# Optimization experiments

Hardware: AMD Instinct MI355X
Metric: run time of the kernel (lower is better)

The kernel has to match this reference:

```python
import jax, jax.numpy as jnp
import numpy as np

B, C, H, W = 8, 64, 128, 128
NH, OPH = 4, 16
MX, MY = 32, 17  # n_modes=(32,32) -> modes_y = 32//2+1
NPAT_S, NPAT_F = 10000, 5000
ED_S, ED_F = 64, 32


def setup_inputs() -> dict:
    ks = jax.random.split(jax.random.key(0), 16)
    n = lambda k, s, sc=1.0: jax.random.normal(k, s, dtype=jnp.float32) * sc
    z = lambda s: jnp.zeros(s, jnp.float32)
    return dict(
        x=n(ks[0], (B, C, H, W)),
        se_emb=n(ks[1], (NPAT_S, ED_S)),
        se_w=n(ks[2], (ED_S, C), 0.1), se_b=z(C),
        mhf_wr=n(ks[3], (NH, C, OPH, MX, MY), 0.01),
        mhf_wi=n(ks[4], (NH, C, OPH, MX, MY), 0.01),
        mhf_bias=z(C),
        sp_emb=n(ks[5], (NPAT_F, ED_F)),
        sp_wr=n(ks[6], (ED_F, C * MX * MY), 0.05), sp_br=z(C * MX * MY),
        sp_wi=n(ks[7], (ED_F, C * MX * MY), 0.05), sp_bi=z(C * MX * MY),
        gate_w1=n(ks[8], (3 * C, 64), 0.05), gate_b1=z(64),
        gate_w2=n(ks[9], (64, 3), 0.05), gate_b2=z(3),
        skip_w=n(ks[10], (C, C), 0.05), skip_b=z(C),
        norm_g=jnp.ones(C), norm_b=z(C),
        mlp_w1=n(ks[11], (C, 2 * C), 0.05), mlp_b1=z(2 * C),
        mlp_w2=n(ks[12], (2 * C, C), 0.05), mlp_b2=z(C),
    )


def _gelu(v):
    return jax.nn.gelu(v, approximate=False)


def _block(x, se_emb, se_w, se_b, mhf_wr, mhf_wi, mhf_bias, sp_emb, sp_wr, sp_br,
           sp_wi, sp_bi, gate_w1, gate_b1, gate_w2, gate_b2, skip_w, skip_b,
           norm_g, norm_b, mlp_w1, mlp_b1, mlp_w2, mlp_b2):
    Bq, Cq, Hq, Wq = x.shape
    # --- SpatialEngram: quantization is elementwise, so sum over window entries
    # equals 3x3 box-sum of the quantized padded field (identical integers,
    # avoids materializing the (B,C,H,W,3,3) unfold tensor).
    xp = jnp.pad(x, ((0, 0), (0, 0), (1, 1), (1, 1)), mode='edge')
    q = (xp * 100.0).astype(jnp.int32)  # trunc toward zero, same as torch .long()
    hv = jnp.zeros((Bq, Cq, Hq, Wq), jnp.int32)
    for i in range(3):
        for j in range(3):
            hv = hv + q[:, :, i:i + Hq, j:j + Wq]
    idx = (jnp.abs(hv) % NPAT_S).astype(jnp.float32).mean(axis=1).astype(jnp.int32)  # (B,H,W)
    spatial = jnp.moveaxis(se_emb[idx] @ se_w + se_b, -1, 1)  # (B,C,H,W)
    # --- MHF multi-head spectral conv (all heads in one einsum; concat == reshape)
    xf = jnp.fft.rfft2(x, norm='ortho')          # (B,C,H,W//2+1) complex64
    lo = xf[:, :, :MX, :MY]
    wc = (mhf_wr + 1j * mhf_wi).astype(lo.dtype)
    of = jnp.einsum('biXY,hioXY->bhoXY', lo, wc).reshape(Bq, Cq, MX, MY)
    full = jnp.zeros((Bq, Cq, Hq, Wq // 2 + 1), lo.dtype).at[:, :, :MX, :MY].set(of)
    mhf = jnp.fft.irfft2(full, s=(Hq, Wq), norm='ortho') + mhf_bias[:, None, None]
    # --- SpectralEngram: per-sample hash of low-freq magnitude -> embedding -> freq proj
    mag = jnp.abs(lo).mean(axis=(1, 2, 3))                       # (B,)
    fidx = (mag * 1000.0).astype(jnp.int32) % NPAT_F
    fe = sp_emb[fidx]                                            # (B,ED_F)
    re = (fe @ sp_wr + sp_br).reshape(Bq, Cq, MX, MY)
    im = (fe @ sp_wi + sp_bi).reshape(Bq, Cq, MX, MY)
    full2 = jnp.zeros((Bq, Cq, Hq, Wq // 2 + 1), lo.dtype).at[:, :, :MX, :MY].set(re + 1j * im)
    spec = jnp.fft.irfft2(full2, s=(Hq, Wq), norm='ortho')
    # --- gated fusion
    gate_in = jnp.concatenate([spatial.mean((2, 3)), mhf.mean((2, 3)), spec.mean((2, 3))], axis=-1)
    gw = jax.nn.softmax(_gelu(gate_in @ gate_w1 + gate_b1) @ gate_w2 + gate_b2, axis=-1)
    a = gw[:, 0, None, None, None]
    bt = gw[:, 1, None, None, None]
    gm = gw[:, 2, None, None, None]
    fused = a * spatial + bt * mhf + gm * spec
    y = fused + jnp.einsum('bihw,io->bohw', x, skip_w) + skip_b[:, None, None]
    # --- GroupNorm(1,C) + 1x1-conv channel MLP (dropout=0)
    mu = y.mean((1, 2, 3), keepdims=True)
    var = y.var((1, 2, 3), keepdims=True)
    yn = (y - mu) * jax.lax.rsqrt(var + 1e-5) * norm_g[:, None, None] + norm_b[:, None, None]
    h = _gelu(jnp.einsum('bihw,io->bohw', yn, mlp_w1) + mlp_b1[:, None, None])
    h = jnp.einsum('bihw,io->bohw', h, mlp_w2) + mlp_b2[:, None, None]
    return y + h


def reference(x, se_emb, se_w, se_b, mhf_wr, mhf_wi, mhf_bias, sp_emb, sp_wr, sp_br,
              sp_wi, sp_bi, gate_w1, gate_b1, gate_w2, gate_b2, skip_w, skip_b,
              norm_g, norm_b, mlp_w1, mlp_b1, mlp_w2, mlp_b2):
    return _block(x, se_emb, se_w, se_b, mhf_wr, mhf_wi, mhf_bias, sp_emb, sp_wr, sp_br,
                  sp_wi, sp_bi, gate_w1, gate_b1, gate_w2, gate_b2, skip_w, skip_b,
                  norm_g, norm_b, mlp_w1, mlp_b1, mlp_w2, mlp_b2)
```

## Files before the change

### kernel.cpp

```cpp
#include <hip/hip_runtime.h>
#include <hip/hip_bf16.h>
#include <math.h>

#define B_ 8
#define C_ 64
#define H_ 128
#define W_ 128
#define NH_ 4
#define OPH_ 16
#define MX_ 32
#define MY_ 17
#define NPAT_F 5000
#define ED_F 32
#define XY_ (MX_*MY_)
#define HW_ (H_*W_)
#define NE_ (B_*C_*H_*W_)

#define OFF_LO     0u
#define OFF_T1     2228224u
#define OFF_T2     2228224u
#define OFF_FMHF   11141120u
#define OFF_FSPEC  13369344u
#define OFF_IDX    33030144u

typedef __hip_bfloat16 bf16;

template<typename T>
__device__ __forceinline__ float ldt(const void* p, int i){ return (float)(((const T*)p)[i]); }

template<typename T>
__device__ __forceinline__ float2 ld2(const void* p, int i){
  if(sizeof(T)==4) return *(const float2*)((const float*)p + i);
  unsigned raw = *(const unsigned*)((const unsigned short*)p + i);
  return make_float2(__uint_as_float(raw<<16), __uint_as_float(raw & 0xffff0000u));
}

__device__ __forceinline__ float gelu_f(float a){
  return 0.5f*a*(1.0f + erff(a*0.70710678118654752f));
}

__device__ __forceinline__ int detect_f32(const void* ng){
  return (((const unsigned*)ng)[0] == 0x3F800000u) ? 1 : 0;
}

template<typename T>
__device__ __forceinline__ void hash_body(const void* x, int* idx, int b, int h, int w){
  int hm = h>0 ? h-1 : 0, hp = h<127 ? h+1 : 127;
  int wm = w>0 ? w-1 : 0, wp = w<127 ? w+1 : 127;
  int s = 0;
  for(int c=0;c<C_;++c){
    const int base = ((b*C_+c)*H_)*W_;
    const int r0 = base + hm*W_, r1 = base + h*W_, r2 = base + hp*W_;
    int q = (int)(ldt<T>(x,r0+wm)*100.0f) + (int)(ldt<T>(x,r0+w)*100.0f) + (int)(ldt<T>(x,r0+wp)*100.0f)
          + (int)(ldt<T>(x,r1+wm)*100.0f) + (int)(ldt<T>(x,r1+w)*100.0f) + (int)(ldt<T>(x,r1+wp)*100.0f)
          + (int)(ldt<T>(x,r2+wm)*100.0f) + (int)(ldt<T>(x,r2+w)*100.0f) + (int)(ldt<T>(x,r2+wp)*100.0f);
    s += (q < 0 ? -q : q) % 10000;
  }
  idx[(b*H_+h)*W_+w] = s >> 6;
}

__global__ __launch_bounds__(256) void k_xprep(const void* __restrict__ x, double* __restrict__ t1,
                                               const void* ng, double* __restrict__ dmag,
                                               float* __restrict__ smean, float* __restrict__ ssum,
                                               float* __restrict__ ssq, int* __restrict__ idx){
  __shared__ float4 xs4[2048];
  __shared__ double2 csd[128];
  int t = threadIdx.x;
  int bid = blockIdx.x;
  int f = detect_f32(ng);
  if(bid == 0){
    if(t < 8){ dmag[t] = 0.0; ssum[t] = 0.f; ssq[t] = 0.f; }
    smean[t] = 0.f; smean[t+256] = 0.f;
  }
  if(bid < 1024){
    if(t<128){ double a = (double)t * (6.283185307179586476925286766559/128.0); csd[t] = make_double2(cos(a), sin(a)); }
    int h0 = (bid & 1) << 6, bcl = bid >> 1;
    long xbase = ((long)bcl*H_ + h0)*W_;
    if(f){
      const float4* xp = (const float4*)((const float*)x + xbase);
      for(int i=t;i<2048;i+=256){
        int r=i>>5, s=i&31;
        xs4[(r<<5) + (s ^ (r&31))] = xp[i];
      }
    } else {
      const uint2* xp = (const uint2*)((const unsigned short*)x + xbase);
      for(int i=t;i<2048;i+=256){
        int r=i>>5, s=i&31;
        uint2 raw = xp[i];
        xs4[(r<<5) + (s ^ (r&31))] = make_float4(
          __uint_as_float(raw.x<<16), __uint_as_float(raw.x & 0xffff0000u),
          __uint_as_float(raw.y<<16), __uint_as_float(raw.y & 0xffff0000u));
      }
    }
    __syncthreads();
    for(int o=t;o<MY_*64;o+=256){
      int ky = o>>6, hr = o&63;
      const float4* xr = xs4 + (hr<<5);
      const int sx = hr & 31;
      double ar=0.0, ai=0.0;
      int m = 0;
      for(int s=0;s<32;++s){
        float4 v4 = xr[s ^ sx];
        double2 c0 = csd[m]; ar = fma((double)v4.x, c0.x, ar); ai = fma(-(double)v4.x, c0.y, ai); m=(m+ky)&127;
        double2 c1 = csd[m]; ar = fma((double)v4.y, c1.x, ar); ai = fma(-(double)v4.y, c1.y, ai); m=(m+ky)&127;
        double2 c2 = csd[m]; ar = fma((double)v4.z, c2.x, ar); ai = fma(-(double)v4.z, c2.y, ai); m=(m+ky)&127;
        double2 c3 = csd[m]; ar = fma((double)v4.w, c3.x, ar); ai = fma(-(double)v4.w, c3.y, ai); m=(m+ky)&127;
      }
      long tt = ((long)(bcl*MY_ + ky))*H_ + (h0 + hr);
      *(double2*)(t1 + 2*tt) = make_double2(ar, ai);
    }
  } else {
    int hb = bid - 1024;
    int b = hb >> 6, h = ((hb & 63) << 1) + (t >> 7), w = t & 127;
    if(f) hash_body<float>(x, idx, b, h, w); else hash_body<bf16>(x, idx, b, h, w);
  }
}

__global__ __launch_bounds__(576) void k_f2m(const double* __restrict__ t1, float* __restrict__ lo,
                                             double* __restrict__ dmag){
  __shared__ double2 ts[MY_*129];
  __shared__ double2 csd[128];
  __shared__ double sred[9];
  int t = threadIdx.x;
  if(t<128){ double a = (double)t * (6.283185307179586476925286766559/128.0); csd[t] = make_double2(cos(a), sin(a)); }
  int bcl = blockIdx.x;
  const double2* tg = (const double2*)t1 + (size_t)bcl*MY_*H_;
  for(int i=t;i<MY_*H_;i+=576){ int ky=i>>7, hh=i&127; ts[ky*129+hh] = tg[i]; }
  __syncthreads();
  double s = 0.0;
  if(t < 544){
    int ky = t % MY_, kx = t / MY_;
    const double2* tr = ts + ky*129;
    double ar=0.0, ai=0.0;
    int m = 0;
    for(int h=0;h<H_;++h){
      double2 v = tr[h];
      double2 cs2 = csd[m];
      double vr = v.x, vi = v.y;
      double cc = cs2.x, ss = cs2.y;
      ar += vr*cc + vi*ss;
      ai += vi*cc - vr*ss;
      m = (m + kx) & 127;
    }
    int g = bcl*XY_ + kx*MY_ + ky;
    float fr = (float)(ar*(1.0/128.0)), fi = (float)(ai*(1.0/128.0));
    *(float2*)(lo + 2*g) = make_float2(fr, fi);
    double re = (double)fr, im = (double)fi;
    s = sqrt(re*re + im*im);
  }
  for(int off=32; off; off>>=1) s += __shfl_down(s, off);
  if((t & 63) == 0) sred[t >> 6] = s;
  __syncthreads();
  if(t == 0){
    double tot = 0.0;
    #pragma unroll
    for(int i=0;i<9;++i) tot += sred[i];
    atomicAdd(&dmag[bcl >> 6], tot);
  }
}

template<typename T>
__device__ __forceinline__ void spatial_load_w(const void* se_w, const void* se_b, float wsm[64][64], float* sb, int t){
  for(int i=t;i<4096;i+=256) wsm[i>>6][i&63] = ldt<T>(se_w, i);
  if(t<64) sb[t] = ldt<T>(se_b, t);
}
template<typename T>
__device__ __forceinline__ void spatial_load_emb(const void* se_emb, const int* ibs, float* emb, int w0, int t){
  for(int i=t;i<2048;i+=256){ int wl_=i>>6, e=i&63; emb[wl_*68 + e] = ldt<T>(se_emb, ibs[w0+wl_]*64 + e); }
}
__global__ __launch_bounds__(256) void k_spatial(const void* se_emb, const void* se_w, const void* se_b,
                                                 const int* __restrict__ idx, bf16* __restrict__ spatial,
                                                 float* __restrict__ smean, const void* ng){
  __shared__ float wsm[64][64];
  __shared__ float emb[32*68];
  __shared__ float sb[64];
  __shared__ int ibs[128];
  int b = blockIdx.x >> 7, h = blockIdx.x & 127, t = threadIdx.x;
  int f = detect_f32(ng);
  if(f) spatial_load_w<float>(se_w, se_b, wsm, sb, t); else spatial_load_w<bf16>(se_w, se_b, wsm, sb, t);
  if(t<128) ibs[t] = idx[(b*H_+h)*W_ + t];
  __syncthreads();
  const int tx = t & 15, ty = t >> 4;
  const int c0 = ty << 2;
  float gsum[4] = {0.f, 0.f, 0.f, 0.f};
  for(int chunk=0; chunk<4; ++chunk){
    int w0 = chunk*32;
    if(f) spatial_load_emb<float>(se_emb, ibs, emb, w0, t); else spatial_load_emb<bf16>(se_emb, ibs, emb, w0, t);
    __syncthreads();
    float acc0[4], acc1[4];
    #pragma unroll
    for(int j=0;j<4;++j){ acc0[j]=sb[c0+j]; acc1[j]=sb[c0+j]; }
    #pragma unroll
    for(int e=0;e<64;e+=4){
      float4 ea = *(const float4*)(emb + tx*68 + e);
      float4 eb = *(const float4*)(emb + (tx+16)*68 + e);
      float ea4[4] = {ea.x, ea.y, ea.z, ea.w};
      float eb4[4] = {eb.x, eb.y, eb.z, eb.w};
      #pragma unroll
      for(int d=0;d<4;++d){
        float4 wv = *(const float4*)(&wsm[e+d][c0]);
        float w4[4] = {wv.x, wv.y, wv.z, wv.w};
        #pragma unroll
        for(int j=0;j<4;++j){
          acc0[j] = fmaf(ea4[d], w4[j], acc0[j]);
          acc1[j] = fmaf(eb4[d], w4[j], acc1[j]);
        }
      }
    }
    #pragma unroll
    for(int j=0;j<4;++j){
      int cc = c0 + j;
      int gb = ((b*C_+cc)*H_+h)*W_ + w0;
      bf16 v0 = __float2bfloat16(acc0[j]);
      bf16 v1 = __float2bfloat16(acc1[j]);
      spatial[gb + tx]      = v0;
      spatial[gb + tx + 16] = v1;
      gsum[j] += __bfloat162float(v0) + __bfloat162float(v1);
    }
    __syncthreads();
  }
  #pragma unroll
  for(int j=0;j<4;++j){
    float g2 = gsum[j];
    g2 += __shfl_xor(g2, 1); g2 += __shfl_xor(g2, 2);
    g2 += __shfl_xor(g2, 4); g2 += __shfl_xor(g2, 8);
    if(tx == 0) atomicAdd(&smean[b*C_ + c0 + j], g2 * (1.0f/16384.0f));
  }
}

template<typename T>
__device__ __forceinline__ void mhf_body(const float* lp, const void* wr, const void* wi,
                                         float* fmhf, int b, int co){
  int hh = co >> 4, o = co & 15;
  for(int xy = threadIdx.x; xy < XY_; xy += 256){
    float ar=0.f, ai=0.f;
    for(int i=0;i<C_;++i){
      float2 l2 = *(const float2*)(lp + (i*XY_+xy)*2);
      float lr = l2.x, li = l2.y;
      int widx = ((hh*C_ + i)*OPH_ + o)*XY_ + xy;
      float wre = ldt<T>(wr, widx), wim = ldt<T>(wi, widx);
      ar += lr*wre - li*wim;
      ai += lr*wim + li*wre;
    }
    int oo = (b*C_ + co)*XY_ + xy;
    *(float2*)(fmhf + 2*oo) = make_float2(ar, ai);
  }
}
template<typename T>
__device__ __forceinline__ void specf_body(const void* sp_emb, const void* sp_wr, const void* sp_br,
                                           const void* sp_wi, const void* sp_bi, const double* dmag,
                                           float* fspec, float* fe, int b, int j0, int t){
  double mag = dmag[b] / (double)(C_*XY_);
  int fv = ((int)(mag*1000.0)) % NPAT_F;
  fv = fv < 0 ? 0 : (fv >= NPAT_F ? NPAT_F-1 : fv);
  if(t < ED_F) fe[t] = ldt<T>(sp_emb, fv*ED_F + t);
  __syncthreads();
  float2 rr = ld2<T>(sp_br, j0), ii = ld2<T>(sp_bi, j0);
  float re0=rr.x, re1=rr.y, im0=ii.x, im1=ii.y;
  #pragma unroll 8
  for(int e=0;e<ED_F;++e){
    float f = fe[e];
    float2 wr = ld2<T>(sp_wr, e*(C_*XY_)+j0);
    float2 wi = ld2<T>(sp_wi, e*(C_*XY_)+j0);
    re0 = fmaf(f, wr.x, re0); im0 = fmaf(f, wi.x, im0);
    re1 = fmaf(f, wr.y, re1); im1 = fmaf(f, wi.y, im1);
  }
  int o = b*C_*XY_ + j0;
  *(float4*)(fspec + 2*o) = make_float4(re0, im0, re1, im1);
}
__global__ __launch_bounds__(256) void k_msf(const float* __restrict__ lo, const void* wr, const void* wi,
                                             float* __restrict__ fmhf,
                                             const void* sp_emb, const void* sp_wr, const void* sp_br,
                                             const void* sp_wi, const void* sp_bi,
                                             const double* __restrict__ dmag,
                                             float* __restrict__ fspec, const void* ng){
  __shared__ float fe[ED_F];
  int bid = blockIdx.x;
  int f = detect_f32(ng);
  if(bid < 512){
    int xcd = bid & 7, slot = bid >> 3;
    int co = (xcd << 3) + (slot & 7);
    int b  = slot >> 3;
    const float* lp = lo + b*C_*XY_*2;
    if(f) mhf_body<float>(lp, wr, wi, fmhf, b, co); else mhf_body<bf16>(lp, wr, wi, fmhf, b, co);
  } else {
    int sidx = bid - 512;
    int b = sidx / 68;
    int j0 = ((sidx % 68)*256 + threadIdx.x)*2;
    if(f) specf_body<float>(sp_emb, sp_wr, sp_br, sp_wi, sp_bi, dmag, fspec, fe, b, j0, threadIdx.x);
    else  specf_body<bf16 >(sp_emb, sp_wr, sp_br, sp_wi, sp_bi, dmag, fspec, fe, b, j0, threadIdx.x);
  }
}

template<typename T>
__device__ __forceinline__ void gate_calc(const float* smean, const float* fmhf, const float* fspec,
                                          const void* mbias, const void* w1, const void* b1,
                                          const void* w2, const void* b2,
                                          float* gin, float* hid, float* gwsh, int b, int t){
  if(t < 64){
    gin[t]      = smean[b*C_+t];
    gin[64+t]   = fmhf [(b*C_+t)*XY_*2] * (1.0f/128.0f) + ldt<T>(mbias, t);
    gin[128+t]  = fspec[(b*C_+t)*XY_*2] * (1.0f/128.0f);
  }
  __syncthreads();
  if(t < 64){
    float acc = ldt<T>(b1, t);
    for(int k=0;k<192;++k) acc = fmaf(gin[k], ldt<T>(w1, k*64+t), acc);
    hid[t] = gelu_f(acc);
  }
  __syncthreads();
  if(t==0){
    float o[3];
    for(int j=0;j<3;++j){
      float a = ldt<T>(b2, j);
      for(int k=0;k<64;++k) a += hid[k]*ldt<T>(w2, k*3+j);
      o[j]=a;
    }
    float mx = fmaxf(o[0], fmaxf(o[1], o[2]));
    float e0=expf(o[0]-mx), e1=expf(o[1]-mx), e2=expf(o[2]-mx);
    float sum=e0+e1+e2;
    gwsh[0]=e0/sum; gwsh[1]=e1/sum; gwsh[2]=e2/sum;
  }
}
__global__ __launch_bounds__(256) void k_comb(const float* __restrict__ fmhf, const float* __restrict__ fspec,
                                              const float* __restrict__ smean, const void* mbias,
                                              const void* gw1, const void* gb1, const void* gw2, const void* gb2,
                                              float* __restrict__ gw, float* __restrict__ t2, const void* ng){
  __shared__ float Gr[XY_], Gi[XY_], cs[128], sn[128];
  __shared__ float gin[192];
  __shared__ float hid[64];
  __shared__ float gwsh[3];
  int c = blockIdx.x, b = blockIdx.y, t = threadIdx.x;
  int f = detect_f32(ng);
  if(t<128) __sincosf((float)t * 0.04908738521234052f, &sn[t], &cs[t]);
  if(f) gate_calc<float>(smean, fmhf, fspec, mbias, gw1, gb1, gw2, gb2, gin, hid, gwsh, b, t);
  else  gate_calc<bf16 >(smean, fmhf, fspec, mbias, gw1, gb1, gw2, gb2, gin, hid, gwsh, b, t);
  __syncthreads();
  float bt=gwsh[1], gm=gwsh[2];
  if(c==0 && t<3) gw[b*3+t] = gwsh[t];
  for(int i=t;i<XY_;i+=256){
    int o = ((b*C_+c)*XY_+i)*2;
    float2 fm = *(const float2*)(fmhf + o);
    float2 fs = *(const float2*)(fspec + o);
    Gr[i] = bt*fm.x + gm*fs.x;
    Gi[i] = bt*fm.y + gm*fs.y;
  }
  __syncthreads();
  const int hh = t & 127;
  float cr[32], sr[32];
  #pragma unroll
  for(int kx=0;kx<MX_;++kx){ int m=(kx*hh)&127; cr[kx]=cs[m]; sr[kx]=sn[m]; }
  for(int i=t;i<MY_*H_;i+=256){
    int ky = i >> 7;
    float ar=0.f, ai=0.f;
    #pragma unroll 8
    for(int kx=0;kx<MX_;++kx){
      float fr=Gr[kx*MY_+ky], fi=Gi[kx*MY_+ky];
      ar += fr*cr[kx] - fi*sr[kx];
      ai += fr*sr[kx] + fi*cr[kx];
    }
    int e = (((b*C_+c)*MY_+ky)*H_ + hh)*2;
    *(float2*)(t2 + e) = make_float2(ar, ai);
  }
}

template<typename T>
__device__ __forceinline__ void fuse_body(const void* x, const void* skw, const void* skb, const void* mbias,
                                          bf16* sp_y, const float* t2, const float* gw,
                                          float* ssum, float* ssq,
                                          float wl[64][64], float* Ur0, float (*UrT)[16], float (*UiT)[16],
                                          float* cs, float* sn, float* sb, float* mb,
                                          float* s1, float* s2, int b, int h, int t){
  int w = t & 127, half = t >> 7;
  if(t<128) __sincosf((float)t * 0.04908738521234052f, &sn[t], &cs[t]);
  for(int i=t;i<4096;i+=256) wl[i>>6][i&63] = ldt<T>(skw, i);
  if(t<64){ sb[t]=ldt<T>(skb,t); mb[t]=ldt<T>(mbias,t); }
  for(int i=t;i<C_*MY_;i+=256){
    int cc=i/MY_, ky=i%MY_;
    int e = (((b*C_+cc)*MY_+ky)*H_ + h)*2;
    float2 v = *(const float2*)(t2 + e);
    if(ky==0){ Ur0[cc]=v.x; }
    else { UrT[cc][ky-1]=v.x; UiT[cc][ky-1]=v.y; }
  }
  float ga=gw[b*3], gbv=gw[b*3+1];
  __syncthreads();
  float cw[MY_], sw[MY_];
  #pragma unroll
  for(int ky=1;ky<MY_;++ky){ int m=(ky*w)&127; cw[ky]=cs[m]; sw[ky]=sn[m]; }
  int c0 = half*32;
  float acc[32];
  #pragma unroll
  for(int j=0;j<32;++j) acc[j]=sb[c0+j];
  int xb = (b*C_*H_ + h)*W_ + w;
  for(int k=0;k<64;++k){
    float xv = ldt<T>(x, xb + k*HW_);
    #pragma unroll
    for(int j=0;j<32;++j) acc[j] = fmaf(xv, wl[k][c0+j], acc[j]);
  }
  float ls=0.f, lq=0.f;
  for(int j=0;j<32;++j){
    int cc=c0+j;
    float vr = Ur0[cc];
    float4 ur0 = *(const float4*)(&UrT[cc][0]);
    float4 ur1 = *(const float4*)(&UrT[cc][4]);
    float4 ur2 = *(const float4*)(&UrT[cc][8]);
    float4 ur3 = *(const float4*)(&UrT[cc][12]);
    float4 ui0 = *(const float4*)(&UiT[cc][0]);
    float4 ui1 = *(const float4*)(&UiT[cc][4]);
    float4 ui2 = *(const float4*)(&UiT[cc][8]);
    float4 ui3 = *(const float4*)(&UiT[cc][12]);
    vr += 2.0f*(ur0.x*cw[1]  - ui0.x*sw[1]);
    vr += 2.0f*(ur0.y*cw[2]  - ui0.y*sw[2]);
    vr += 2.0f*(ur0.z*cw[3]  - ui0.z*sw[3]);
    vr += 2.0f*(ur0.w*cw[4]  - ui0.w*sw[4]);
    vr += 2.0f*(ur1.x*cw[5]  - ui1.x*sw[5]);
    vr += 2.0f*(ur1.y*cw[6]  - ui1.y*sw[6]);
    vr += 2.0f*(ur1.z*cw[7]  - ui1.z*sw[7]);
    vr += 2.0f*(ur1.w*cw[8]  - ui1.w*sw[8]);
    vr += 2.0f*(ur2.x*cw[9]  - ui2.x*sw[9]);
    vr += 2.0f*(ur2.y*cw[10] - ui2.y*sw[10]);
    vr += 2.0f*(ur2.z*cw[11] - ui2.z*sw[11]);
    vr += 2.0f*(ur2.w*cw[12] - ui2.w*sw[12]);
    vr += 2.0f*(ur3.x*cw[13] - ui3.x*sw[13]);
    vr += 2.0f*(ur3.y*cw[14] - ui3.y*sw[14]);
    vr += 2.0f*(ur3.z*cw[15] - ui3.z*sw[15]);
    vr += 2.0f*(ur3.w*cw[16] - ui3.w*sw[16]);
    int gi = ((b*C_+cc)*H_+h)*W_+w;
    float v = ga*__bfloat162float(sp_y[gi]) + vr*(1.0f/128.0f) + gbv*mb[cc] + acc[j];
    sp_y[gi] = __float2bfloat16(v);
    ls += v; lq = fmaf(v, v, lq);
  }
  s1[t]=ls; s2[t]=lq; __syncthreads();
  for(int k=128;k>0;k>>=1){ if(t<k){ s1[t]+=s1[t+k]; s2[t]+=s2[t+k]; } __syncthreads(); }
  if(t==0){ atomicAdd(&ssum[b], s1[0]); atomicAdd(&ssq[b], s2[0]); }
}
__global__ __launch_bounds__(256) void k_fuse(const void* x, const void* skw, const void* skb, const void* mbias,
                                              bf16* __restrict__ sp_y, const float* __restrict__ t2,
                                              const float* __restrict__ gw,
                                              float* __restrict__ ssum, float* __restrict__ ssq, const void* ng){
  __shared__ float wl[64][64];
  __shared__ float Ur0[64];
  __shared__ float UrT[64][16], UiT[64][16];
  __shared__ float cs[128], sn[128];
  __shared__ float sb[64], mb[64];
  __shared__ float s1[256], s2[256];
  int h = blockIdx.x, b = blockIdx.y, t = threadIdx.x;
  int f = detect_f32(ng);
  if(f) fuse_body<float>(x, skw, skb, mbias, sp_y, t2, gw, ssum, ssq, wl, Ur0, UrT, UiT, cs, sn, sb, mb, s1, s2, b, h, t);
  else  fuse_body<bf16 >(x, skw, skb, mbias, sp_y, t2, gw, ssum, ssq, wl, Ur0, UrT, UiT, cs, sn, sb, mb, s1, s2, b, h, t);
}

template<typename T>
__device__ __forceinline__ void mlp_body(const bf16* __restrict__ y, float mu, float rs,
                                         const void* ng, const void* nb, const void* w1, const void* b1,
                                         const void* w2, const void* b2, float* __restrict__ out,
                                         float* __restrict__ yn_s, float* __restrict__ w_s,
                                         int b, int h, int t){
  const int tx = t & 15, ty = t >> 4;
  const int pA = tx << 2, pB = 64 + (tx << 2);
  const int ybase = (b*C_*H_ + h)*W_;

  #pragma unroll
  for(int jj=0;jj<16;++jj) w_s[t + (jj<<8)] = ldt<T>(w1, t + (jj<<8));
  for(int it=0; it<8; ++it){
    int chunk = t + (it<<8);
    int c = chunk >> 5, p4 = (chunk & 31) << 2;
    const unsigned short* yp = (const unsigned short*)y + ybase + c*HW_ + p4;
    uint2 raw = *(const uint2*)yp;
    float g = ldt<T>(ng, c), nbv = ldt<T>(nb, c);
    float sc = rs*g;
    float4 o;
    o.x = (__uint_as_float(raw.x<<16)          - mu)*sc + nbv;
    o.y = (__uint_as_float(raw.x & 0xffff0000u)- mu)*sc + nbv;
    o.z = (__uint_as_float(raw.y<<16)          - mu)*sc + nbv;
    o.w = (__uint_as_float(raw.y & 0xffff0000u)- mu)*sc + nbv;
    *(float4*)(yn_s + c*132 + p4) = o;
  }
  float pf[16];
  #pragma unroll
  for(int jj=0;jj<16;++jj) pf[jj] = ldt<T>(w1, 4096 + t + (jj<<8));
  __syncthreads();

  const int kA = ty << 2, kB = 64 + (ty << 2);
  float a[8][8];
  #pragma unroll
  for(int j=0;j<4;++j){
    float bj = ldt<T>(b1, kA+j);
    float bj2 = ldt<T>(b1, kB+j);
    #pragma unroll
    for(int q=0;q<8;++q){ a[j][q]=bj; a[4+j][q]=bj2; }
  }
  #pragma unroll 4
  for(int i=0;i<32;++i){
    float4 y1 = *(const float4*)(yn_s + i*132 + pA);
    float4 y2 = *(const float4*)(yn_s + i*132 + pB);
    float4 wa = *(const float4*)(w_s + (i<<7) + kA);
    float4 wb = *(const float4*)(w_s + (i<<7) + kB);
    float y8[8] = {y1.x,y1.y,y1.z,y1.w,y2.x,y2.y,y2.z,y2.w};
    float w8[8] = {wa.x,wa.y,wa.z,wa.w,wb.x,wb.y,wb.z,wb.w};
    #pragma unroll
    for(int j=0;j<8;++j){
      #pragma unroll
      for(int q=0;q<8;++q) a[j][q] = fmaf(y8[q], w8[j], a[j][q]);
    }
  }
  __syncthreads();
  #pragma unroll
  for(int jj=0;jj<16;++jj) w_s[t + (jj<<8)] = pf[jj];
  #pragma unroll
  for(int jj=0;jj<16;++jj) pf[jj] = ldt<T>(w2, t + (jj<<8));
  __syncthreads();
  #pragma unroll 4
  for(int i=0;i<32;++i){
    float4 y1 = *(const float4*)(yn_s + (32+i)*132 + pA);
    float4 y2 = *(const float4*)(yn_s + (32+i)*132 + pB);
    float4 wa = *(const float4*)(w_s + (i<<7) + kA);
    float4 wb = *(const float4*)(w_s + (i<<7) + kB);
    float y8[8] = {y1.x,y1.y,y1.z,y1.w,y2.x,y2.y,y2.z,y2.w};
    float w8[8] = {wa.x,wa.y,wa.z,wa.w,wb.x,wb.y,wb.z,wb.w};
    #pragma unroll
    for(int j=0;j<8;++j){
      #pragma unroll
      for(int q=0;q<8;++q) a[j][q] = fmaf(y8[q], w8[j], a[j][q]);
    }
  }
  __syncthreads();
  #pragma unroll
  for(int jj=0;jj<16;++jj) w_s[t + (jj<<8)] = pf[jj];
  #pragma unroll
  for(int jj=0;jj<16;++jj) pf[jj] = ldt<T>(w2, 4096 + t + (jj<<8));
  #pragma unroll
  for(int j=0;j<4;++j){
    float4 h1, h2;
    h1.x = gelu_f(a[j][0]); h1.y = gelu_f(a[j][1]); h1.z = gelu_f(a[j][2]); h1.w = gelu_f(a[j][3]);
    h2.x = gelu_f(a[j][4]); h2.y = gelu_f(a[j][5]); h2.z = gelu_f(a[j][6]); h2.w = gelu_f(a[j][7]);
    *(float4*)(yn_s + (kA+j)*132 + pA) = h1;
    *(float4*)(yn_s + (kA+j)*132 + pB) = h2;
  }
  __syncthreads();

  const int c0 = ty << 2;
  float acc[4][8];
  #pragma unroll
  for(int j=0;j<4;++j){
    #pragma unroll
    for(int q=0;q<8;++q) acc[j][q] = 0.f;
  }
  #pragma unroll 4
  for(int k=0;k<64;++k){
    float4 h1 = *(const float4*)(yn_s + k*132 + pA);
    float4 h2 = *(const float4*)(yn_s + k*132 + pB);
    float4 wv = *(const float4*)(w_s + (k<<6) + c0);
    float h8[8] = {h1.x,h1.y,h1.z,h1.w,h2.x,h2.y,h2.z,h2.w};
    float w4[4] = {wv.x, wv.y, wv.z, wv.w};
    #pragma unroll
    for(int j=0;j<4;++j){
      #pragma unroll
      for(int q=0;q<8;++q) acc[j][q] = fmaf(h8[q], w4[j], acc[j][q]);
    }
  }
  __syncthreads();
  #pragma unroll
  for(int jj=0;jj<16;++jj) w_s[t + (jj<<8)] = pf[jj];
  #pragma unroll
  for(int j=0;j<4;++j){
    float4 h1, h2;
    h1.x = gelu_f(a[4+j][0]); h1.y = gelu_f(a[4+j][1]); h1.z = gelu_f(a[4+j][2]); h1.w = gelu_f(a[4+j][3]);
    h2.x = gelu_f(a[4+j][4]); h2.y = gelu_f(a[4+j][5]); h2.z = gelu_f(a[4+j][6]); h2.w = gelu_f(a[4+j][7]);
    *(float4*)(yn_s + (kA+j)*132 + pA) = h1;
    *(float4*)(yn_s + (kA+j)*132 + pB) = h2;
  }
  __syncthreads();
  #pragma unroll 4
  for(int k=0;k<64;++k){
    float4 h1 = *(const float4*)(yn_s + k*132 + pA);
    float4 h2 = *(const float4*)(yn_s + k*132 + pB);
    float4 wv = *(const float4*)(w_s + (k<<6) + c0);
    float h8[8] = {h1.x,h1.y,h1.z,h1.w,h2.x,h2.y,h2.z,h2.w};
    float w4[4] = {wv.x, wv.y, wv.z, wv.w};
    #pragma unroll
    for(int j=0;j<4;++j){
      #pragma unroll
      for(int q=0;q<8;++q) acc[j][q] = fmaf(h8[q], w4[j], acc[j][q]);
    }
  }

  #pragma unroll
  for(int j=0;j<4;++j){
    int c = c0 + j;
    float b2v = ldt<T>(b2, c);
    const unsigned short* yp1 = (const unsigned short*)y + ybase + c*HW_ + pA;
    const unsigned short* yp2 = (const unsigned short*)y + ybase + c*HW_ + pB;
    uint2 r1 = *(const uint2*)yp1;
    uint2 r2 = *(const uint2*)yp2;
    float4 o1, o2;
    o1.x = __uint_as_float(r1.x<<16)           + acc[j][0] + b2v;
    o1.y = __uint_as_float(r1.x & 0xffff0000u) + acc[j][1] + b2v;
    o1.z = __uint_as_float(r1.y<<16)           + acc[j][2] + b2v;
    o1.w = __uint_as_float(r1.y & 0xffff0000u) + acc[j][3] + b2v;
    o2.x = __uint_as_float(r2.x<<16)           + acc[j][4] + b2v;
    o2.y = __uint_as_float(r2.x & 0xffff0000u) + acc[j][5] + b2v;
    o2.z = __uint_as_float(r2.y<<16)           + acc[j][6] + b2v;
    o2.w = __uint_as_float(r2.y & 0xffff0000u) + acc[j][7] + b2v;
    *(float4*)(out + ybase + c*HW_ + pA) = o1;
    *(float4*)(out + ybase + c*HW_ + pB) = o2;
  }
}
__global__ __launch_bounds__(256) void k_mlp(const bf16* __restrict__ y, const float* __restrict__ ssum,
                                             const float* __restrict__ ssq, const void* ng, const void* nb,
                                             const void* w1, const void* b1, const void* w2, const void* b2,
                                             float* __restrict__ out){
  __shared__ float yn_s[64*132];
  __shared__ float w_s[4096];
  int h = blockIdx.x, b = blockIdx.y;
  int t = threadIdx.x;
  float m = ssum[b] * (1.0f/1048576.0f);
  float v = ssq[b] * (1.0f/1048576.0f) - m*m;
  float rs = rsqrtf(v + 1e-5f);
  int f = detect_f32(ng);
  if(f) mlp_body<float>(y, m, rs, ng, nb, w1, b1, w2, b2, out, yn_s, w_s, b, h, t);
  else  mlp_body<bf16 >(y, m, rs, ng, nb, w1, b1, w2, b2, out, yn_s, w_s, b, h, t);
}

extern "C" void kernel_launch(void* const* d_in, const int* in_sizes, int n_in,
                              void* d_out, int out_size, void* d_ws, size_t ws_size,
                              hipStream_t stream) {
  (void)out_size; (void)ws_size;
  static const int dict_sizes[24] = {8388608,640000,4096,64,2228224,2228224,64,160000,
                                     1114112,34816,1114112,34816,12288,64,192,3,
                                     4096,64,64,64,8192,128,8192,64};
  static const int sorted_sizes[24] = {64,3,12288,192,64,2228224,2228224,128,64,8192,8192,
                                       64,64,64,640000,4096,64,4096,34816,34816,160000,
                                       1114112,1114112,8388608};
  static const int sorted_to_dict[24] = {13,15,12,14,6,5,4,21,23,20,22,19,18,3,1,2,17,16,11,9,7,10,8,0};

  const void* in[24];
  bool is_dict = (n_in == 24), is_sorted = (n_in == 24);
  if(n_in == 24){
    for(int i=0;i<24;++i){
      if(in_sizes[i] != dict_sizes[i])   is_dict   = false;
      if(in_sizes[i] != sorted_sizes[i]) is_sorted = false;
    }
  }
  if(is_sorted && !is_dict){
    for(int i=0;i<24;++i) in[sorted_to_dict[i]] = d_in[i];
  } else {
    for(int i=0;i<24 && i<n_in;++i) in[i] = d_in[i];
  }

  const void* x       = in[0];
  const void* se_emb  = in[1];
  const void* se_w    = in[2];
  const void* se_b    = in[3];
  const void* mhf_wr  = in[4];
  const void* mhf_wi  = in[5];
  const void* mhf_bias= in[6];
  const void* sp_emb  = in[7];
  const void* sp_wr   = in[8];
  const void* sp_br   = in[9];
  const void* sp_wi   = in[10];
  const void* sp_bi   = in[11];
  const void* gate_w1 = in[12];
  const void* gate_b1 = in[13];
  const void* gate_w2 = in[14];
  const void* gate_b2 = in[15];
  const void* skip_w  = in[16];
  const void* skip_b  = in[17];
  const void* norm_g  = in[18];
  const void* norm_b  = in[19];
  const void* mlp_w1  = in[20];
  const void* mlp_b1  = in[21];
  const void* mlp_w2  = in[22];
  const void* mlp_b2  = in[23];
  float* out = (float*)d_out;

  bf16*   sp_y = (bf16*)d_ws;
  float*  scal = (float*)((char*)d_ws + (size_t)NE_*2);
  float* smean = scal;
  float* gw    = scal + 512;
  float* ssum  = scal + 536;
  float* ssq   = scal + 544;
  double* dmag = (double*)(scal + 584);

  char* ob = (char*)d_out;
  float*  lo    = (float*) (ob + OFF_LO);
  double* t1    = (double*)(ob + OFF_T1);
  float*  t2    = (float*) (ob + OFF_T2);
  float*  fmhf  = (float*) (ob + OFF_FMHF);
  float*  fspec = (float*) (ob + OFF_FSPEC);
  int*    idx   = (int*)   (ob + OFF_IDX);

  hipLaunchKernelGGL(k_xprep,  dim3(1536),       dim3(256), 0, stream, x, t1, norm_g, dmag, smean, ssum, ssq, idx);
  hipLaunchKernelGGL(k_f2m,    dim3(512),        dim3(576), 0, stream, t1, lo, dmag);
  hipLaunchKernelGGL(k_spatial,dim3(B_*H_),      dim3(256), 0, stream, se_emb, se_w, se_b, idx, sp_y, smean, norm_g);
  hipLaunchKernelGGL(k_msf,    dim3(1056),       dim3(256), 0, stream, lo, mhf_wr, mhf_wi, fmhf, sp_emb, sp_wr, sp_br, sp_wi, sp_bi, dmag, fspec, norm_g);
  hipLaunchKernelGGL(k_comb,   dim3(C_, B_),     dim3(256), 0, stream, fmhf, fspec, smean, mhf_bias, gate_w1, gate_b1, gate_w2, gate_b2, gw, t2, norm_g);
  hipLaunchKernelGGL(k_fuse,   dim3(H_, B_),     dim3(256), 0, stream, x, skip_w, skip_b, mhf_bias, sp_y, t2, gw, ssum, ssq, norm_g);
  hipLaunchKernelGGL(k_mlp,    dim3(H_, B_),     dim3(256), 0, stream, sp_y, ssum, ssq, norm_g, norm_b, mlp_w1, mlp_b1, mlp_w2, mlp_b2, out);
}
```

Measured before the change: 434.0 us.

## Merge spatial-embedding kernel into spectral launch and split gate MLP into own kernel

Folds the spatial-embedding GEMM blocks into the same launch as the MHF and spectral-feature blocks, so the three independent workloads share one grid and can overlap instead of running back to back. The gate MLP, which every k_comb block used to recompute redundantly, moves to a tiny per-batch kernel, and k_comb just reads the gate weights. This adds one small launch and raises shared-memory use in the merged kernel, because every block now reserves the spatial buffers, which may reduce occupancy for the MHF and spectral blocks.

```diff
diff --git a/kernel.cpp b/kernel.cpp
--- a/kernel.cpp
+++ b/kernel.cpp
@@ -168,16 +168,12 @@
 __device__ __forceinline__ void spatial_load_emb(const void* se_emb, const int* ibs, float* emb, int w0, int t){
   for(int i=t;i<2048;i+=256){ int wl_=i>>6, e=i&63; emb[wl_*68 + e] = ldt<T>(se_emb, ibs[w0+wl_]*64 + e); }
 }
-__global__ __launch_bounds__(256) void k_spatial(const void* se_emb, const void* se_w, const void* se_b,
-                                                 const int* __restrict__ idx, bf16* __restrict__ spatial,
-                                                 float* __restrict__ smean, const void* ng){
-  __shared__ float wsm[64][64];
-  __shared__ float emb[32*68];
-  __shared__ float sb[64];
-  __shared__ int ibs[128];
-  int b = blockIdx.x >> 7, h = blockIdx.x & 127, t = threadIdx.x;
-  int f = detect_f32(ng);
-  if(f) spatial_load_w<float>(se_w, se_b, wsm, sb, t); else spatial_load_w<bf16>(se_w, se_b, wsm, sb, t);
+template<typename T>
+__device__ __forceinline__ void spatial_body(const void* se_emb, const void* se_w, const void* se_b,
+                                             const int* idx, bf16* spatial, float* smean,
+                                             float wsm[64][64], float* emb, float* sb, int* ibs,
+                                             int b, int h, int t){
+  spatial_load_w<T>(se_w, se_b, wsm, sb, t);
   if(t<128) ibs[t] = idx[(b*H_+h)*W_ + t];
   __syncthreads();
   const int tx = t & 15, ty = t >> 4;
@@ -185,7 +181,7 @@
   float gsum[4] = {0.f, 0.f, 0.f, 0.f};
   for(int chunk=0; chunk<4; ++chunk){
     int w0 = chunk*32;
-    if(f) spatial_load_emb<float>(se_emb, ibs, emb, w0, t); else spatial_load_emb<bf16>(se_emb, ibs, emb, w0, t);
+    spatial_load_emb<T>(se_emb, ibs, emb, w0, t);
     __syncthreads();
     float acc0[4], acc1[4];
     #pragma unroll
@@ -268,23 +264,36 @@
   int o = b*C_*XY_ + j0;
   *(float4*)(fspec + 2*o) = make_float4(re0, im0, re1, im1);
 }
-__global__ __launch_bounds__(256) void k_msf(const float* __restrict__ lo, const void* wr, const void* wi,
-                                             float* __restrict__ fmhf,
-                                             const void* sp_emb, const void* sp_wr, const void* sp_br,
-                                             const void* sp_wi, const void* sp_bi,
-                                             const double* __restrict__ dmag,
-                                             float* __restrict__ fspec, const void* ng){
+
+__global__ __launch_bounds__(256) void k_sm(const void* se_emb, const void* se_w, const void* se_b,
+                                            const int* __restrict__ idx, bf16* __restrict__ spatial,
+                                            float* __restrict__ smean,
+                                            const float* __restrict__ lo, const void* wr, const void* wi,
+                                            float* __restrict__ fmhf,
+                                            const void* sp_emb, const void* sp_wr, const void* sp_br,
+                                            const void* sp_wi, const void* sp_bi,
+                                            const double* __restrict__ dmag,
+                                            float* __restrict__ fspec, const void* ng){
+  __shared__ float wsm[64][64];
+  __shared__ float emb[32*68];
+  __shared__ float sb[64];
+  __shared__ int ibs[128];
   __shared__ float fe[ED_F];
   int bid = blockIdx.x;
   int f = detect_f32(ng);
-  if(bid < 512){
-    int xcd = bid & 7, slot = bid >> 3;
+  if(bid < 1024){
+    int b = bid >> 7, h = bid & 127;
+    if(f) spatial_body<float>(se_emb, se_w, se_b, idx, spatial, smean, wsm, emb, sb, ibs, b, h, threadIdx.x);
+    else  spatial_body<bf16 >(se_emb, se_w, se_b, idx, spatial, smean, wsm, emb, sb, ibs, b, h, threadIdx.x);
+  } else if(bid < 1536){
+    int mbid = bid - 1024;
+    int xcd = mbid & 7, slot = mbid >> 3;
     int co = (xcd << 3) + (slot & 7);
     int b  = slot >> 3;
     const float* lp = lo + b*C_*XY_*2;
     if(f) mhf_body<float>(lp, wr, wi, fmhf, b, co); else mhf_body<bf16>(lp, wr, wi, fmhf, b, co);
   } else {
-    int sidx = bid - 512;
+    int sidx = bid - 1536;
     int b = sidx / 68;
     int j0 = ((sidx % 68)*256 + threadIdx.x)*2;
     if(f) specf_body<float>(sp_emb, sp_wr, sp_br, sp_wi, sp_bi, dmag, fspec, fe, b, j0, threadIdx.x);
@@ -293,21 +302,17 @@
 }
 
 template<typename T>
-__device__ __forceinline__ void gate_calc(const float* smean, const float* fmhf, const float* fspec,
+__device__ __forceinline__ void gate_body(const float* smean, const float* fmhf, const float* fspec,
                                           const void* mbias, const void* w1, const void* b1,
                                           const void* w2, const void* b2,
-                                          float* gin, float* hid, float* gwsh, int b, int t){
-  if(t < 64){
-    gin[t]      = smean[b*C_+t];
-    gin[64+t]   = fmhf [(b*C_+t)*XY_*2] * (1.0f/128.0f) + ldt<T>(mbias, t);
-    gin[128+t]  = fspec[(b*C_+t)*XY_*2] * (1.0f/128.0f);
-  }
-  __syncthreads();
-  if(t < 64){
-    float acc = ldt<T>(b1, t);
-    for(int k=0;k<192;++k) acc = fmaf(gin[k], ldt<T>(w1, k*64+t), acc);
-    hid[t] = gelu_f(acc);
-  }
+                                          float* gw, float* gin, float* hid, int b, int t){
+  gin[t]      = smean[b*C_+t];
+  gin[64+t]   = fmhf [(b*C_+t)*XY_*2] * (1.0f/128.0f) + ldt<T>(mbias, t);
+  gin[128+t]  = fspec[(b*C_+t)*XY_*2] * (1.0f/128.0f);
+  __syncthreads();
+  float acc = ldt<T>(b1, t);
+  for(int k=0;k<192;++k) acc = fmaf(gin[k], ldt<T>(w1, k*64+t), acc);
+  hid[t] = gelu_f(acc);
   __syncthreads();
   if(t==0){
     float o[3];
@@ -319,25 +324,27 @@
     float mx = fmaxf(o[0], fmaxf(o[1], o[2]));
     float e0=expf(o[0]-mx), e1=expf(o[1]-mx), e2=expf(o[2]-mx);
     float sum=e0+e1+e2;
-    gwsh[0]=e0/sum; gwsh[1]=e1/sum; gwsh[2]=e2/sum;
-  }
-}
-__global__ __launch_bounds__(256) void k_comb(const float* __restrict__ fmhf, const float* __restrict__ fspec,
-                                              const float* __restrict__ smean, const void* mbias,
-                                              const void* gw1, const void* gb1, const void* gw2, const void* gb2,
-                                              float* __restrict__ gw, float* __restrict__ t2, const void* ng){
-  __shared__ float Gr[XY_], Gi[XY_], cs[128], sn[128];
+    gw[b*3+0]=e0/sum; gw[b*3+1]=e1/sum; gw[b*3+2]=e2/sum;
+  }
+}
+__global__ __launch_bounds__(64) void k_gate(const float* __restrict__ smean, const float* __restrict__ fmhf,
+                                             const float* __restrict__ fspec, const void* mbias,
+                                             const void* w1, const void* b1, const void* w2, const void* b2,
+                                             float* __restrict__ gw, const void* ng){
   __shared__ float gin[192];
   __shared__ float hid[64];
-  __shared__ float gwsh[3];
+  int b = blockIdx.x, t = threadIdx.x;
+  int f = detect_f32(ng);
+  if(f) gate_body<float>(smean, fmhf, fspec, mbias, w1, b1, w2, b2, gw, gin, hid, b, t);
+  else  gate_body<bf16 >(smean, fmhf, fspec, mbias, w1, b1, w2, b2, gw, gin, hid, b, t);
+}
+
+__global__ __launch_bounds__(256) void k_comb(const float* __restrict__ fmhf, const float* __restrict__ fspec,
+                                              const float* __restrict__ gw, float* __restrict__ t2){
+  __shared__ float Gr[XY_], Gi[XY_], cs[128], sn[128];
   int c = blockIdx.x, b = blockIdx.y, t = threadIdx.x;
-  int f = detect_f32(ng);
   if(t<128) __sincosf((float)t * 0.04908738521234052f, &sn[t], &cs[t]);
-  if(f) gate_calc<float>(smean, fmhf, fspec, mbias, gw1, gb1, gw2, gb2, gin, hid, gwsh, b, t);
-  else  gate_calc<bf16 >(smean, fmhf, fspec, mbias, gw1, gb1, gw2, gb2, gin, hid, gwsh, b, t);
-  __syncthreads();
-  float bt=gwsh[1], gm=gwsh[2];
-  if(c==0 && t<3) gw[b*3+t] = gwsh[t];
+  float bt=gw[b*3+1], gm=gw[b*3+2];
   for(int i=t;i<XY_;i+=256){
     int o = ((b*C_+c)*XY_+i)*2;
     float2 fm = *(const float2*)(fmhf + o);
@@ -692,9 +699,9 @@
 
   hipLaunchKernelGGL(k_xprep,  dim3(1536),       dim3(256), 0, stream, x, t1, norm_g, dmag, smean, ssum, ssq, idx);
   hipLaunchKernelGGL(k_f2m,    dim3(512),        dim3(576), 0, stream, t1, lo, dmag);
-  hipLaunchKernelGGL(k_spatial,dim3(B_*H_),      dim3(256), 0, stream, se_emb, se_w, se_b, idx, sp_y, smean, norm_g);
-  hipLaunchKernelGGL(k_msf,    dim3(1056),       dim3(256), 0, stream, lo, mhf_wr, mhf_wi, fmhf, sp_emb, sp_wr, sp_br, sp_wi, sp_bi, dmag, fspec, norm_g);
-  hipLaunchKernelGGL(k_comb,   dim3(C_, B_),     dim3(256), 0, stream, fmhf, fspec, smean, mhf_bias, gate_w1, gate_b1, gate_w2, gate_b2, gw, t2, norm_g);
+  hipLaunchKernelGGL(k_sm,     dim3(2080),       dim3(256), 0, stream, se_emb, se_w, se_b, idx, sp_y, smean, lo, mhf_wr, mhf_wi, fmhf, sp_emb, sp_wr, sp_br, sp_wi, sp_bi, dmag, fspec, norm_g);
+  hipLaunchKernelGGL(k_gate,   dim3(B_),         dim3(64),  0, stream, smean, fmhf, fspec, mhf_bias, gate_w1, gate_b1, gate_w2, gate_b2, gw, norm_g);
+  hipLaunchKernelGGL(k_comb,   dim3(C_, B_),     dim3(256), 0, stream, fmhf, fspec, gw, t2);
   hipLaunchKernelGGL(k_fuse,   dim3(H_, B_),     dim3(256), 0, stream, x, skip_w, skip_b, mhf_bias, sp_y, t2, gw, ssum, ssq, norm_g);
   hipLaunchKernelGGL(k_mlp,    dim3(H_, B_),     dim3(256), 0, stream, sp_y, ssum, ssq, norm_g, norm_b, mlp_w1, mlp_b1, mlp_w2, mlp_b2, out);
 }
```

Measured after the change: 418.9 us. 1.04x faster.
